# Performance work log

Hardware: AMD Instinct MI355X
Metric: run time of the kernel (lower is better)

Reference implementation:

```python
import jax, jax.numpy as jnp
import numpy as np

# --- static config (matches init_kwargs) ---
N = 30000            # n_nodes
H = 8                # num_heads
OT = 16              # out_time_dim
OS = 240             # out_space_dim
IN_DIM = 16 + 1 + 240   # in_time+1 + in_space = 257
OUT_DIM = OT + 1 + OS   # 257 per head
BETA = -1.0
EPS = 1e-8
MAX_NORM = 1.0e6
SQRT_BETA = float(np.sqrt(abs(BETA)))


def setup_inputs() -> dict:
    key = jax.random.key(0)
    ks = jax.random.split(key, 7)
    def w(k, shape, fan_in):
        return (jax.random.normal(k, shape, jnp.float32) / np.sqrt(fan_in)).astype(jnp.float32)
    return {
        "query_input": jax.random.normal(ks[0], (N, IN_DIM), jnp.float32),
        "source_input": jax.random.normal(ks[1], (N, IN_DIM), jnp.float32),
        # stacked per-head PseudoLinear2 weights: [H, out, in]
        "Wq": w(ks[2], (H, OUT_DIM, IN_DIM), IN_DIM),
        "Wk": w(ks[3], (H, OUT_DIM, IN_DIM), IN_DIM),
        "Wv": w(ks[4], (H, OUT_DIM, IN_DIM), IN_DIM),
        # final head-concat projections (nn.Linear, bias=False): [out, in]
        "Ws": w(ks[5], (OT + 1, H * (OT + 1)), H * (OT + 1)),
        "Wh": w(ks[6], (OS, H * OS), H * OS),
    }


def _pseudo_linear(x, W):
    # Per-head linear; spherical block renormalized to radius sqrt(|beta|)
    # (hr output on the product manifold S^OT x H^OS). [N,D] x [H,O,D] -> [N,H,O]
    y = jnp.einsum('nd,hod->nho', x, W)
    s, sp = y[..., :OT + 1], y[..., OT + 1:]
    s = s * (SQRT_BETA / (jnp.linalg.norm(s, axis=-1, keepdims=True) + EPS))
    return jnp.concatenate([s, sp], axis=-1)


def _linear_attention(q, k, v, den_eps):
    # elu+1 feature-map linear attention; associative kv outer product per head.
    phi_q = jax.nn.elu(q) + 1.0
    phi_k = jax.nn.elu(k) + 1.0
    ktv = jnp.einsum('nhm,nhd->hmd', phi_k, v)          # [H,m,d]
    num = jnp.einsum('nhm,hmd->nhd', phi_q, ktv)        # [N,H,d]
    den = jnp.einsum('nhd,hd->nh', phi_q, phi_k.sum(0)) # [N,H]
    return num / (den[..., None] + den_eps)


def _l2norm(x):
    # torch F.normalize(p=2, dim=-1)
    return x / jnp.clip(jnp.linalg.norm(x, axis=-1, keepdims=True), 1e-12)


def reference(query_input, source_input, Wq, Wk, Wv, Ws, Wh):
    q = _pseudo_linear(query_input, Wq)   # [N,H,257]
    k = _pseudo_linear(source_input, Wk)
    v = _pseudo_linear(source_input, Wv)
    qs, qh = q[..., :OT + 1], q[..., OT + 1:]
    ks_, kh = k[..., :OT + 1], k[..., OT + 1:]
    vs, vh = v[..., :OT + 1], v[..., OT + 1:]

    # ---- spherical linear attention ----
    a = _linear_attention(qs, ks_, vs, 1e-6)            # [N,H,OT+1]
    a = a.reshape(N, H * (OT + 1)) @ Ws.T               # heads_concat
    an = jnp.linalg.norm(a, axis=-1, keepdims=True) + EPS
    mask = (an > MAX_NORM).astype(a.dtype)
    an_c = jnp.minimum(an, MAX_NORM)
    a_ = (a / an_c) * mask + a * (1.0 - mask)
    att_s = SQRT_BETA * _l2norm(a_)                     # [N,OT+1]

    # ---- hyperbolic linear attention ----
    b = _linear_attention(qh, kh, vh, 1e-8)             # [N,H,OS]
    b = b.reshape(N, H * OS) @ Wh.T
    bn = jnp.linalg.norm(b, axis=-1, keepdims=True) + EPS
    maskb = (bn > MAX_NORM).astype(b.dtype)
    bn_c = jnp.minimum(bn, MAX_NORM)
    b_ = _l2norm(b / bn_c) * MAX_NORM
    b2 = b_ * maskb + b * (1.0 - maskb)
    bt = jnp.sqrt(bn_c ** 2 - BETA)                     # hyperbolic time coord
    att_h = jnp.concatenate([bt, b2], axis=-1)          # [N,OS+1]

    out = jnp.concatenate([att_s, att_h], axis=-1)      # [N,OT+1+OS+1]
    # sh_to_q: product S x H -> pseudo-hyperboloid Q; reverse_extrinsic_map = identity here.
    s_part, h_part = out[:, :OT + 1], out[:, OT + 1:]
    q_out = jnp.concatenate([h_part[:, :1] * s_part / SQRT_BETA, h_part[:, 1:]], axis=-1)
    return q_out  # [N, 257]
```

## Files before the change

### kernel.cpp

```cpp
#include <hip/hip_runtime.h>
#include <math.h>

typedef __bf16 bf16_t;
typedef __bf16 bf16x8 __attribute__((ext_vector_type(8)));
typedef float f32x4 __attribute__((ext_vector_type(4)));

#define H    8
#define SD   17
#define HD   240
#define KIN  257
#define KQP  288
#define SCOL 256
#define DTOT 2176
#define NTOT 30000
#define CHS  6000
#define NCS  5
#define CHPS 6144
#define CHQ  7500
#define CHQP 7552
#define NCQ  4
#define KSPLIT 16

#define BK   32

__device__ __forceinline__ float phi_elu1(float x) {
    return x > 0.f ? x + 1.f : __expf(x);
}

__device__ __forceinline__ int xcd_swz(int orig, int nwg) {
    int q = nwg >> 3, r = nwg & 7;
    int xcd = orig & 7, off = orig >> 3;
    return (xcd < r ? xcd * (q + 1) : r * (q + 1) + (xcd - r) * q) + off;
}

__device__ __forceinline__ void gl_lds16(const bf16_t* g, bf16_t* l) {
    __builtin_amdgcn_global_load_lds(
        (const __attribute__((address_space(1))) void*)g,
        (__attribute__((address_space(3))) void*)l, 16, 0, 0);
}

template<int N> __device__ __forceinline__ void waitvm() {
    asm volatile("s_waitcnt vmcnt(%0)" :: "n"(N) : "memory");
    __builtin_amdgcn_sched_barrier(0);
}

struct GemmP {
    const bf16_t* A; long lda; long aHead;
    const bf16_t* B; long ldb; long bHead;
    float* Cf; bf16_t* Cb; long ldc; long cHead; int atomicC;
    int M, N, K, nSplit;
};

template<int TBM, int TBN>
__global__ void __launch_bounds__(256)
k_mfma_nt(GemmP p)
{
    constexpr int FI = TBM / 32;
    constexpr int FJ = TBN / 32;
    constexpr int LPT = TBM / 64 + TBN / 64;
    __shared__ bf16_t As[3][TBM * BK];
    __shared__ bf16_t Bs[3][TBN * BK];
    const int t  = threadIdx.x;
    const int z  = blockIdx.z;
    const int h  = z / p.nSplit;
    const int sp = z % p.nSplit;
    const int kWin = p.K / p.nSplit;
    const int k0   = sp * kWin;
    const int nwg  = gridDim.x * gridDim.y;
    const int wg   = xcd_swz(blockIdx.y * gridDim.x + blockIdx.x, nwg);
    const int m0 = (wg % gridDim.x) * TBM;
    const int n0 = (wg / gridDim.x) * TBN;
    const bf16_t* A = p.A + (long)h * p.aHead;
    const bf16_t* B = p.B + (long)h * p.bHead;

    const int lr = t >> 2;
    const int lc = t & 3;
    const int wid  = t >> 6;
    const int lane = t & 63;
    const int wm = (wid >> 1) * (TBM / 2);
    const int wn = (wid & 1) * (TBN / 2);
    const int fr = lane & 15;
    const int fq = lane >> 4;

    f32x4 acc[FI][FJ] = {};

    auto stage = [&](int buf, int kb) {
        const int gk = kb + ((lc ^ ((lr >> 1) & 3)) << 3);
#pragma unroll
        for (int it = 0; it < TBM / 64; ++it)
            gl_lds16(A + (long)(m0 + lr + it * 64) * p.lda + gk, &As[buf][it * 2048 + t * 8]);
#pragma unroll
        for (int it = 0; it < TBN / 64; ++it)
            gl_lds16(B + (long)(n0 + lr + it * 64) * p.ldb + gk, &Bs[buf][it * 2048 + t * 8]);
    };

    const int nSteps = kWin / BK;
    stage(0, k0);
    if (nSteps > 1) stage(1, k0 + BK);
    int cur = 0, pf = 2;
#pragma unroll 1
    for (int s = 0; s < nSteps; ++s) {
        if (s + 1 < nSteps) waitvm<LPT>();
        else                waitvm<0>();
        __builtin_amdgcn_s_barrier();
        __builtin_amdgcn_sched_barrier(0);
        if (s + 2 < nSteps) {
            stage(pf, k0 + (s + 2) * BK);
            pf = (pf == 2) ? 0 : pf + 1;
        }
        bf16x8 af[FI], bfr[FJ];
#pragma unroll
        for (int i = 0; i < FI; ++i) {
            const int row = wm + i * 16 + fr;
            af[i] = *(const bf16x8*)(&As[cur][row * BK + ((fq ^ ((row >> 1) & 3)) << 3)]);
        }
#pragma unroll
        for (int j = 0; j < FJ; ++j) {
            const int row = wn + j * 16 + fr;
            bfr[j] = *(const bf16x8*)(&Bs[cur][row * BK + ((fq ^ ((row >> 1) & 3)) << 3)]);
        }
#pragma unroll
        for (int i = 0; i < FI; ++i)
#pragma unroll
            for (int j = 0; j < FJ; ++j)
                acc[i][j] = __builtin_amdgcn_mfma_f32_16x16x32_bf16(af[i], bfr[j], acc[i][j], 0, 0, 0);
        cur = (cur == 2) ? 0 : cur + 1;
    }

    float*  Cf = p.Cf ? p.Cf + (long)h * p.cHead : (float*)0;
    bf16_t* Cb = p.Cb ? p.Cb + (long)h * p.cHead : (bf16_t*)0;
#pragma unroll
    for (int i = 0; i < FI; ++i) {
#pragma unroll
        for (int r = 0; r < 4; ++r) {
            const int m = m0 + wm + i * 16 + fq * 4 + r;
            if (m >= p.M) continue;
#pragma unroll
            for (int j = 0; j < FJ; ++j) {
                const int n = n0 + wn + j * 16 + fr;
                if (n >= p.N) continue;
                const float v = acc[i][j][r];
                const long idx = (long)m * p.ldc + n;
                if (p.atomicC)      atomicAdd(&Cf[idx], v);
                else if (Cf)        Cf[idx] = v;
                else                Cb[idx] = (bf16_t)v;
            }
        }
    }
}

__global__ void __launch_bounds__(256)
k_mfma_kv(const bf16_t* __restrict__ A, const bf16_t* __restrict__ Bsrc,
          bf16_t* __restrict__ Tk, bf16_t* __restrict__ Tv,
          float* __restrict__ ksum, int nRows)
{
    constexpr int FI = 4, FJ = 4;
    constexpr int LPT = 4;
    __shared__ bf16_t As[3][128 * BK];
    __shared__ bf16_t Bs[3][128 * BK];
    const int t = threadIdx.x;
    const int nwg = gridDim.x * gridDim.y;
    const int wg  = xcd_swz(blockIdx.y * gridDim.x + blockIdx.x, nwg);
    const int m0 = (wg % gridDim.x) * 128;
    const int n0 = (wg / gridDim.x) * 128;

    const int lr = t >> 2;
    const int lc = t & 3;
    const int wid  = t >> 6;
    const int lane = t & 63;
    const int wm = (wid >> 1) * 64;
    const int wn = (wid & 1) * 64;
    const int fr = lane & 15;
    const int fq = lane >> 4;

    f32x4 acc[FI][FJ] = {};

    auto stage = [&](int buf, int kb) {
        const int gk = kb + ((lc ^ ((lr >> 1) & 3)) << 3);
        gl_lds16(A    + (long)(m0 + lr)      * KQP + gk, &As[buf][t * 8]);
        gl_lds16(A    + (long)(m0 + lr + 64) * KQP + gk, &As[buf][2048 + t * 8]);
        gl_lds16(Bsrc + (long)(n0 + lr)      * KQP + gk, &Bs[buf][t * 8]);
        gl_lds16(Bsrc + (long)(n0 + lr + 64) * KQP + gk, &Bs[buf][2048 + t * 8]);
    };

    constexpr int nSteps = KQP / BK;
    stage(0, 0);
    stage(1, BK);
    int cur = 0, pf = 2;
#pragma unroll 1
    for (int s = 0; s < nSteps; ++s) {
        if (s + 1 < nSteps) waitvm<LPT>();
        else                waitvm<0>();
        __builtin_amdgcn_s_barrier();
        __builtin_amdgcn_sched_barrier(0);
        if (s + 2 < nSteps) {
            stage(pf, (s + 2) * BK);
            pf = (pf == 2) ? 0 : pf + 1;
        }
        bf16x8 af[FI], bfr[FJ];
#pragma unroll
        for (int i = 0; i < FI; ++i) {
            const int row = wm + i * 16 + fr;
            af[i] = *(const bf16x8*)(&As[cur][row * BK + ((fq ^ ((row >> 1) & 3)) << 3)]);
        }
#pragma unroll
        for (int j = 0; j < FJ; ++j) {
            const int row = wn + j * 16 + fr;
            bfr[j] = *(const bf16x8*)(&Bs[cur][row * BK + ((fq ^ ((row >> 1) & 3)) << 3)]);
        }
#pragma unroll
        for (int i = 0; i < FI; ++i)
#pragma unroll
            for (int j = 0; j < FJ; ++j)
                acc[i][j] = __builtin_amdgcn_mfma_f32_16x16x32_bf16(af[i], bfr[j], acc[i][j], 0, 0, 0);
        cur = (cur == 2) ? 0 : cur + 1;
    }

    const bool isKh = (m0 >= SCOL) && (m0 < DTOT);
    bf16_t* outB = (m0 < DTOT) ? (Tk + (long)m0 * CHPS)
                               : (Tv + (long)(m0 - DTOT) * CHPS);
#pragma unroll
    for (int i = 0; i < FI; ++i) {
#pragma unroll
        for (int r = 0; r < 4; ++r) {
            const int ml = wm + i * 16 + fq * 4 + r;
            bf16_t* row = outB + (long)ml * CHPS;
            float kacc = 0.f;
#pragma unroll
            for (int j = 0; j < FJ; ++j) {
                const int n = n0 + wn + j * 16 + fr;
                float v = 0.f;
                if (n < nRows) {
                    v = acc[i][j][r];
                    if (isKh) { v = phi_elu1(v); kacc += v; }
                }
                row[n] = (bf16_t)v;
            }
            if (isKh) {
                kacc += __shfl_xor(kacc, 1);
                kacc += __shfl_xor(kacc, 2);
                kacc += __shfl_xor(kacc, 4);
                kacc += __shfl_xor(kacc, 8);
                if (fr == 0) atomicAdd(&ksum[m0 + ml], kacc);
            }
        }
    }
}

__global__ void k_zero_tail(bf16_t* __restrict__ Tk, bf16_t* __restrict__ Tv)
{
    const int row = blockIdx.x;
    const int t = threadIdx.x;
    bf16_t* B = (t >= 128) ? Tv : Tk;
    B[(long)row * CHPS + (CHPS - 128) + (t & 127)] = (bf16_t)0.f;
}

__global__ void __launch_bounds__(256)
k_post_kv_t(bf16_t* __restrict__ Tk, bf16_t* __restrict__ Tv,
            float* __restrict__ ksum, int rows)
{
    const int h = blockIdx.y;
    const int n = blockIdx.x * 256 + threadIdx.x;
    const int lane = threadIdx.x & 63;
    const bool act = n < rows;
    float kv[SD], vv[SD];
    float sk = 0.f, sv = 0.f;
#pragma unroll
    for (int j = 0; j < SD; ++j) {
        kv[j] = act ? (float)Tk[(long)(h * 32 + j) * CHPS + n] : 0.f;
        vv[j] = act ? (float)Tv[(long)(h * 32 + j) * CHPS + n] : 0.f;
        sk += kv[j] * kv[j];
        sv += vv[j] * vv[j];
    }
    const float ik = 1.f / (sqrtf(sk) + 1e-8f);
    const float iv = 1.f / (sqrtf(sv) + 1e-8f);
#pragma unroll
    for (int j = 0; j < SD; ++j) {
        float pk = act ? phi_elu1(kv[j] * ik) : 0.f;
        if (act) {
            Tk[(long)(h * 32 + j) * CHPS + n] = (bf16_t)pk;
            Tv[(long)(h * 32 + j) * CHPS + n] = (bf16_t)(vv[j] * iv);
        }
        float s = pk;
#pragma unroll
        for (int off = 32; off > 0; off >>= 1) s += __shfl_down(s, off);
        if (lane == 0) atomicAdd(&ksum[h * 32 + j], s);
    }
}

__global__ void k_cast_pad(const float* __restrict__ in, bf16_t* __restrict__ out, long rows)
{
    long i = (long)blockIdx.x * 256 + threadIdx.x;
    if (i >= rows * (KQP / 8)) return;
    long r = i / (KQP / 8); int c8 = (int)(i - r * (KQP / 8)) * 8;
    const float* ip = in + r * KIN + c8;
    bf16x8 o;
#pragma unroll
    for (int j = 0; j < 8; ++j)
        o[j] = (c8 + j < KIN) ? (bf16_t)ip[j] : (bf16_t)0.f;
    *(bf16x8*)(out + r * KQP + c8) = o;
}

__global__ void k_prep_proj(const float* __restrict__ W, bf16_t* __restrict__ dst)
{
    long i = (long)blockIdx.x * 256 + threadIdx.x;
    if (i >= (long)DTOT * KQP) return;
    int r = (int)(i / KQP), k = (int)(i % KQP);
    float v = 0.f;
    if (r < SCOL) {
        int h = r >> 5, j = r & 31;
        if (j < SD && k < KIN) v = W[((long)h * 257 + j) * 257 + k];
    } else {
        int rr = r - SCOL;
        int h = rr / HD, j = rr % HD;
        if (k < KIN) v = W[((long)h * 257 + SD + j) * 257 + k];
    }
    dst[i] = (bf16_t)v;
}

__global__ void k_prep_ws(const float* __restrict__ ws, bf16_t* __restrict__ out)
{
    int o = blockIdx.x; int t = threadIdx.x;
    int h = t >> 5, j = t & 31;
    float v = 0.f;
    if (o < SD && j < SD) v = ws[o * (H * SD) + h * SD + j];
    out[o * 256 + t] = (bf16_t)v;
}

__global__ void k_prep_wh(const float* __restrict__ wh, bf16_t* __restrict__ out)
{
    long i = (long)blockIdx.x * 256 + threadIdx.x;
    if (i >= 256L * 2048) return;
    int o = (int)(i / 2048), c = (int)(i % 2048);
    int h = c >> 8, j = c & 255;
    float v = 0.f;
    if (o < 240 && j < HD) v = wh[(long)o * 1920 + h * HD + j];
    out[i] = (bf16_t)v;
}

__global__ void __launch_bounds__(256)
k_post_q(bf16_t* __restrict__ Yq, const float* __restrict__ ksum, int rows)
{
    const int wid  = blockIdx.x * 4 + (threadIdx.x >> 6);
    const int lane = threadIdx.x & 63;
    const int n = wid >> 3, h = wid & 7;
    if (n >= rows) return;
    bf16_t* row = Yq + (long)n * DTOT;
    float qv = (lane < SD) ? (float)row[h * 32 + lane] : 0.f;
    float sq = qv * qv;
#pragma unroll
    for (int off = 32; off > 0; off >>= 1) sq += __shfl_down(sq, off);
    sq = __shfl(sq, 0);
    const float iq = 1.f / (sqrtf(sq) + 1e-8f);
    float pvs = (lane < SD) ? phi_elu1(qv * iq) : 0.f;
    float ds = (lane < SD) ? pvs * ksum[h * 32 + lane] : 0.f;
    float ph[8];
    float dh = 0.f;
    if (lane < 30) {
        bf16x8 hv8 = *(const bf16x8*)(row + SCOL + h * HD + lane * 8);
        const float* kp = ksum + SCOL + h * HD + lane * 8;
#pragma unroll
        for (int i = 0; i < 8; ++i) {
            ph[i] = phi_elu1((float)hv8[i]);
            dh += ph[i] * kp[i];
        }
    }
#pragma unroll
    for (int off = 32; off > 0; off >>= 1) {
        ds += __shfl_down(ds, off);
        dh += __shfl_down(dh, off);
    }
    ds = __shfl(ds, 0); dh = __shfl(dh, 0);
    const float ss = 1.f / (ds + 1e-6f);
    const float sh = 1.f / (dh + 1e-8f);
    if (lane < 32)
        row[h * 32 + lane] = (bf16_t)((lane < SD) ? pvs * ss : 0.f);
    if (lane < 30) {
        bf16x8 o8;
#pragma unroll
        for (int i = 0; i < 8; ++i) o8[i] = (bf16_t)(ph[i] * sh);
        *(bf16x8*)(row + SCOL + h * HD + lane * 8) = o8;
    }
}

__global__ void k_castf(const float* __restrict__ in, bf16_t* __restrict__ out, long n)
{
    long i = (long)blockIdx.x * 256 + threadIdx.x;
    if (i < n) out[i] = (bf16_t)in[i];
}

__global__ void __launch_bounds__(256)
k_finalize(const float* __restrict__ pre, float* __restrict__ outp, int rows)
{
    int n    = blockIdx.x * 4 + (threadIdx.x >> 6);
    int lane = threadIdx.x & 63;
    if (n >= rows) return;
    const float* rp = pre + (long)n * 257;
    float* op = outp + (long)n * 257;
    float sv = (lane < SD) ? rp[lane] : 0.f;
    float ssq = sv * sv;
    float hv[4];
    float hsq = 0.f;
#pragma unroll
    for (int i = 0; i < 4; ++i) {
        int o = lane + 64 * i;
        hv[i] = (o < HD) ? rp[SD + o] : 0.f;
        hsq += hv[i] * hv[i];
    }
#pragma unroll
    for (int off = 32; off > 0; off >>= 1) {
        ssq += __shfl_down(ssq, off);
        hsq += __shfl_down(hsq, off);
    }
    ssq = __shfl(ssq, 0); hsq = __shfl(hsq, 0);
    float an_raw = sqrtf(ssq);
    float bn_raw = sqrtf(hsq);
    float an = an_raw + 1e-8f;
    float bn = bn_raw + 1e-8f;
    bool ma = an > 1e6f;
    bool mb = bn > 1e6f;
    float an_c = fminf(an, 1e6f);
    float bn_c = fminf(bn, 1e6f);
    float na = ma ? (an_raw / an_c) : an_raw;
    na = fmaxf(na, 1e-12f);
    float inv_s = (ma ? (1.f / an_c) : 1.f) / na;
    float bt = sqrtf(bn_c * bn_c + 1.0f);
    float nb = fmaxf(bn_raw / bn_c, 1e-12f);
    float scale_b = 1e6f / (bn_c * nb);
    if (lane < SD) op[lane] = bt * (sv * inv_s);
#pragma unroll
    for (int i = 0; i < 4; ++i) {
        int o = lane + 64 * i;
        if (o < HD) op[SD + o] = mb ? hv[i] * scale_b : hv[i];
    }
}

static inline long alup(long b) { return (b + 255) & ~255L; }

extern "C" void kernel_launch(void* const* d_in, const int* in_sizes, int n_in,
                              void* d_out, int out_size, void* d_ws, size_t ws_size,
                              hipStream_t stream)
{
    const float* query  = (const float*)d_in[0];
    const float* source = (const float*)d_in[1];
    const float* Wq     = (const float*)d_in[2];
    const float* Wk     = (const float*)d_in[3];
    const float* Wv     = (const float*)d_in[4];
    const float* Ws     = (const float*)d_in[5];
    const float* Wh     = (const float*)d_in[6];
    float* out = (float*)d_out;

    char* p = (char*)d_ws;
    auto alloc = [&](long b) { char* r = p; p += alup(b); return r; };
    bf16_t* Wkvb = (bf16_t*)alloc(2L * DTOT * KQP * 2);
    bf16_t* Wqb  = (bf16_t*)alloc((long)DTOT * KQP * 2);
    bf16_t* Wsb  = (bf16_t*)alloc(64L * 256 * 2);
    bf16_t* Whb  = (bf16_t*)alloc(256L * 2048 * 2);
    bf16_t* Gfull= (bf16_t*)alloc(320L * DTOT * 2);
    float*  ktvF = (float*) alloc((8L * HD * 256 + 8L * 32 * 32) * 4);
    float*  ksum = (float*) alloc((long)DTOT * 4);
    bf16_t* ktvB = (bf16_t*)alloc((8L * HD * 256 + 8L * 32 * 32) * 2);
    bf16_t* xcb  = (bf16_t*)alloc((long)CHQP * KQP * 2);
    long tkBytes = (long)DTOT * CHPS * 2;
    char* ub = alloc(2 * tkBytes + 16L * CHPS * 2);
    bf16_t* Tk  = (bf16_t*)ub;
    bf16_t* Tv  = Tk + (long)DTOT * CHPS;
    bf16_t* Yq  = Tk;
    float*  opre= (float*)(Yq + (long)CHQP * DTOT);

    float*  ktvHf = ktvF;
    float*  ktvSf = ktvF + 8L * HD * 256;
    bf16_t* ktvHb = ktvB;
    bf16_t* ktvSb = ktvB + 8L * HD * 256;

    (void)hipMemsetAsync(ktvF, 0, (char*)(ksum + DTOT) - (char*)ktvF, stream);
    (void)hipMemsetAsync(Gfull, 0, 320L * DTOT * 2, stream);

    const unsigned gw = (unsigned)(((long)DTOT * KQP + 255) / 256);
    k_prep_proj<<<gw, 256, 0, stream>>>(Wk, Wkvb);
    k_prep_proj<<<gw, 256, 0, stream>>>(Wv, Wkvb + (long)DTOT * KQP);
    k_prep_proj<<<gw, 256, 0, stream>>>(Wq, Wqb);
    k_prep_ws<<<64, 256, 0, stream>>>(Ws, Wsb);
    k_prep_wh<<<(unsigned)((256L * 2048 + 255) / 256), 256, 0, stream>>>(Wh, Whb);

    GemmP g;

    k_zero_tail<<<DTOT, 256, 0, stream>>>(Tk, Tv);
    for (int c = 0; c < NCS; ++c) {
        const float* src = source + (long)c * CHS * KIN;
        k_cast_pad<<<(unsigned)(((long)CHS * (KQP / 8) + 255) / 256), 256, 0, stream>>>(src, xcb, CHS);
        k_mfma_kv<<<dim3((2 * DTOT) / 128, (CHS + 127) / 128, 1), 256, 0, stream>>>(
            Wkvb, xcb, Tk, Tv, ksum, CHS);
        k_post_kv_t<<<dim3((CHS + 255) / 256, H), 256, 0, stream>>>(Tk, Tv, ksum, CHS);
        g = { Tk + (long)SCOL * CHPS, CHPS, (long)HD * CHPS,
              Tv + (long)SCOL * CHPS, CHPS, (long)HD * CHPS,
              ktvHf, 0, 256, (long)HD * 256, 1,  HD, HD, CHPS, KSPLIT };
        k_mfma_nt<128, 128><<<dim3(2, 2, H * KSPLIT), 256, 0, stream>>>(g);
        g = { Tk, CHPS, 32L * CHPS,  Tv, CHPS, 32L * CHPS,
              ktvSf, 0, 32, 32L * 32, 1,  32, 32, CHPS, KSPLIT };
        k_mfma_nt<64, 64><<<dim3(1, 1, H * KSPLIT), 256, 0, stream>>>(g);
    }
    k_castf<<<(unsigned)((8L * (HD * 256 + 32 * 32) + 255) / 256), 256, 0, stream>>>(
        ktvF, ktvB, 8L * (HD * 256 + 32 * 32));

    g = { Wsb, 256, 32,  ktvSb, 32, 32L * 32,  0, Gfull, DTOT, 32, 0,
          SD, 32, 32, 1 };
    k_mfma_nt<64, 64><<<dim3(1, 1, H), 256, 0, stream>>>(g);
    g = { Whb, 2048, 256,  ktvHb, 256, (long)HD * 256,
          0, Gfull + 17L * DTOT + SCOL, DTOT, HD, 0,
          HD, HD, 256, 1 };
    k_mfma_nt<64, 64><<<dim3(4, 4, H), 256, 0, stream>>>(g);

    for (int c = 0; c < NCQ; ++c) {
        const float* qsrc = query + (long)c * CHQ * KIN;
        float* orow = out + (long)c * CHQ * 257;
        k_cast_pad<<<(unsigned)(((long)CHQ * (KQP / 8) + 255) / 256), 256, 0, stream>>>(qsrc, xcb, CHQ);
        g = { xcb, KQP, 0,  Wqb, KQP, 0,  0, Yq, DTOT, 0, 0,
              CHQ, DTOT, KQP, 1 };
        k_mfma_nt<128, 128><<<dim3((CHQ + 127) / 128, DTOT / 128, 1), 256, 0, stream>>>(g);
        k_post_q<<<(CHQ * H) / 4, 256, 0, stream>>>(Yq, ksum, CHQ);
        g = { Yq, DTOT, 0,  Gfull, DTOT, 0,  opre, 0, 257, 0, 0,
              CHQ, 257, DTOT, 1 };
        k_mfma_nt<64, 64><<<dim3((CHQ + 63) / 64, 5, 1), 256, 0, stream>>>(g);
        k_finalize<<<(CHQ + 3) / 4, 256, 0, stream>>>(opre, orow, CHQ);
    }
}
```

Baseline: 1.156 ms.

## Split-K the query output GEMM into separate slabs reduced in finalize

The final per-chunk GEMM (Yq × Gfull, K=2176) is split four ways along K, with each split writing its partial result to its own fp32 slab through a new atomicC==3 mode. The finalize kernel then sums the four slabs before applying its normalizations. The tile shape also changes to 64x192 with two N-blocks, which makes Gfull padding grow to 384 rows. This is meant to raise occupancy for a GEMM that had few workgroups and a long K loop. The cost is extra slab memory traffic and a larger workspace.

```diff
diff --git a/kernel.cpp b/kernel.cpp
--- a/kernel.cpp
+++ b/kernel.cpp
@@ -20,6 +20,8 @@
 #define CHQP 7552
 #define NCQ  4
 #define KSPLIT 16
+#define OSPLIT 4
+#define OSLAB (7552L * 257)
 
 #define BK   32
 
@@ -127,8 +129,10 @@
         cur = (cur == 2) ? 0 : cur + 1;
     }
 
-    float*  Cf = p.Cf ? p.Cf + (long)h * p.cHead : (float*)0;
-    bf16_t* Cb = p.Cb ? p.Cb + (long)h * p.cHead : (bf16_t*)0;
+    float*  Cf = 0; bf16_t* Cb = 0;
+    if (p.atomicC == 3)      Cf = p.Cf + (long)z * p.cHead;
+    else if (p.Cf)           Cf = p.Cf + (long)h * p.cHead;
+    else                     Cb = p.Cb + (long)h * p.cHead;
 #pragma unroll
     for (int i = 0; i < FI; ++i) {
 #pragma unroll
@@ -141,9 +145,9 @@
                 if (n >= p.N) continue;
                 const float v = acc[i][j][r];
                 const long idx = (long)m * p.ldc + n;
-                if (p.atomicC)      atomicAdd(&Cf[idx], v);
-                else if (Cf)        Cf[idx] = v;
-                else                Cb[idx] = (bf16_t)v;
+                if (p.atomicC == 1)      atomicAdd(&Cf[idx], v);
+                else if (Cf)             Cf[idx] = v;
+                else                     Cb[idx] = (bf16_t)v;
             }
         }
     }
@@ -397,15 +401,24 @@
     if (n >= rows) return;
     const float* rp = pre + (long)n * 257;
     float* op = outp + (long)n * 257;
-    float sv = (lane < SD) ? rp[lane] : 0.f;
+    float sv = 0.f;
+    if (lane < SD) {
+#pragma unroll
+        for (int s = 0; s < OSPLIT; ++s) sv += rp[s * OSLAB + lane];
+    }
     float ssq = sv * sv;
     float hv[4];
     float hsq = 0.f;
 #pragma unroll
     for (int i = 0; i < 4; ++i) {
         int o = lane + 64 * i;
-        hv[i] = (o < HD) ? rp[SD + o] : 0.f;
-        hsq += hv[i] * hv[i];
+        float v = 0.f;
+        if (o < HD) {
+#pragma unroll
+            for (int s = 0; s < OSPLIT; ++s) v += rp[s * OSLAB + SD + o];
+        }
+        hv[i] = v;
+        hsq += v * v;
     }
 #pragma unroll
     for (int off = 32; off > 0; off >>= 1) {
@@ -456,17 +469,17 @@
     bf16_t* Wqb  = (bf16_t*)alloc((long)DTOT * KQP * 2);
     bf16_t* Wsb  = (bf16_t*)alloc(64L * 256 * 2);
     bf16_t* Whb  = (bf16_t*)alloc(256L * 2048 * 2);
-    bf16_t* Gfull= (bf16_t*)alloc(320L * DTOT * 2);
+    bf16_t* Gfull= (bf16_t*)alloc(384L * DTOT * 2);
     float*  ktvF = (float*) alloc((8L * HD * 256 + 8L * 32 * 32) * 4);
     float*  ksum = (float*) alloc((long)DTOT * 4);
     bf16_t* ktvB = (bf16_t*)alloc((8L * HD * 256 + 8L * 32 * 32) * 2);
     bf16_t* xcb  = (bf16_t*)alloc((long)CHQP * KQP * 2);
+    float*  opre = (float*) alloc(OSPLIT * OSLAB * 4);
     long tkBytes = (long)DTOT * CHPS * 2;
     char* ub = alloc(2 * tkBytes + 16L * CHPS * 2);
     bf16_t* Tk  = (bf16_t*)ub;
     bf16_t* Tv  = Tk + (long)DTOT * CHPS;
     bf16_t* Yq  = Tk;
-    float*  opre= (float*)(Yq + (long)CHQP * DTOT);
 
     float*  ktvHf = ktvF;
     float*  ktvSf = ktvF + 8L * HD * 256;
@@ -474,7 +487,7 @@
     bf16_t* ktvSb = ktvB + 8L * HD * 256;
 
     (void)hipMemsetAsync(ktvF, 0, (char*)(ksum + DTOT) - (char*)ktvF, stream);
-    (void)hipMemsetAsync(Gfull, 0, 320L * DTOT * 2, stream);
+    (void)hipMemsetAsync(Gfull, 0, 384L * DTOT * 2, stream);
 
     const unsigned gw = (unsigned)(((long)DTOT * KQP + 255) / 256);
     k_prep_proj<<<gw, 256, 0, stream>>>(Wk, Wkvb);
@@ -519,9 +532,9 @@
               CHQ, DTOT, KQP, 1 };
         k_mfma_nt<128, 128><<<dim3((CHQ + 127) / 128, DTOT / 128, 1), 256, 0, stream>>>(g);
         k_post_q<<<(CHQ * H) / 4, 256, 0, stream>>>(Yq, ksum, CHQ);
-        g = { Yq, DTOT, 0,  Gfull, DTOT, 0,  opre, 0, 257, 0, 0,
-              CHQ, 257, DTOT, 1 };
-        k_mfma_nt<64, 64><<<dim3((CHQ + 63) / 64, 5, 1), 256, 0, stream>>>(g);
+        g = { Yq, DTOT, 0,  Gfull, DTOT, 0,  opre, 0, 257, OSLAB, 3,
+              CHQ, 257, DTOT, OSPLIT };
+        k_mfma_nt<64, 192><<<dim3((CHQ + 63) / 64, 2, OSPLIT), 256, 0, stream>>>(g);
         k_finalize<<<(CHQ + 3) / 4, 256, 0, stream>>>(opre, orow, CHQ);
     }
 }
```

Measured after the change: 1.170 ms. Within noise of the previous version (+1.2%).
